# Kernel tuning notes

Hardware: AMD Instinct MI355X
Metric: run time of the kernel (lower is better)

The kernel has to match this reference:

```python
import jax, jax.numpy as jnp
import numpy as np

NUM_HEADS = 12
HEAD_DIM = 64  # dim=768 // 12
SCALE = HEAD_DIM ** (-0.5)  # NOTE: original divides q by this -> multiplies by sqrt(head_dim)


def setup_inputs() -> dict:
    key = jax.random.key(0)
    k1, k2, k3 = jax.random.split(key, 3)
    B, N, C = 1, 4096, 768
    x = jax.random.normal(k1, (B, N, C), dtype=jnp.float32)
    qkv_w = jax.random.normal(k2, (3 * C, C), dtype=jnp.float32) * 0.01
    qkv_b = jnp.zeros((3 * C,), dtype=jnp.float32)
    proj_w = jax.random.normal(k3, (C, C), dtype=jnp.float32) * 0.01
    proj_b = jnp.zeros((C,), dtype=jnp.float32)
    return {"x": x, "qkv_w": qkv_w, "qkv_b": qkv_b, "proj_w": proj_w, "proj_b": proj_b}


def reference(x, qkv_w, qkv_b, proj_w, proj_b):
    B, N, C = x.shape
    H, D = NUM_HEADS, HEAD_DIM
    # qkv projection: [B,N,3C]
    qkv = x @ qkv_w.T + qkv_b
    qkv = qkv.reshape(B, N, 3, H, D).transpose(2, 0, 3, 1, 4)  # [3,B,H,N,D]
    q, k, v = qkv[0], qkv[1], qkv[2]
    # Faithful quirk: q / scale with scale = D**-0.5 => logits scaled by sqrt(D)
    attn = jnp.einsum('bhnd,bhmd->bhnm', q / SCALE, k)  # [B,H,N,N]
    attn = jax.nn.softmax(attn, axis=-1)
    # dropout omitted (eval mode / deterministic reference)
    out = jnp.einsum('bhnm,bhmd->bhnd', attn, v)  # [B,H,N,D]
    out = out.transpose(0, 2, 1, 3).reshape(B, N, C)
    out = out @ proj_w.T + proj_b
    return out
```

## Files before the change

### kernel.cpp

```cpp
#include <hip/hip_runtime.h>


typedef short bf16x8 __attribute__((ext_vector_type(8)));
typedef float f32x4 __attribute__((ext_vector_type(4)));
typedef unsigned short u16;
typedef unsigned int u32;

__device__ __forceinline__ u16 f2bf(float f) {
  u32 u = __float_as_uint(f);
  u = (u + 0x7fffu + ((u >> 16) & 1u)) >> 16;
  return (u16)u;
}

__device__ __forceinline__ u32 cvtpk(float a, float b) {
  u32 r;
  asm("v_cvt_pk_bf16_f32 %0, %1, %2" : "=v"(r) : "v"(a), "v"(b));
  return r;
}

__device__ __forceinline__ void gload16(const void* g, void* l) {
  __builtin_amdgcn_global_load_lds(
      (const __attribute__((address_space(1))) unsigned int*)g,
      (__attribute__((address_space(3))) unsigned int*)l, 16, 0, 0);
}

__device__ __forceinline__ void pl32swap(u32& x, u32& y) {
  asm("v_permlane32_swap_b32 %0, %1" : "+v"(x), "+v"(y));
}
__device__ __forceinline__ void pl16swap(u32& x, u32& y) {
  asm("v_permlane16_swap_b32 %0, %1" : "+v"(x), "+v"(y));
}

__global__ void cast3(const float* __restrict__ a, int na4,
                      const float* __restrict__ b, int nb4,
                      const float* __restrict__ c, int nc4,
                      u16* __restrict__ oa, u16* __restrict__ obp, u16* __restrict__ oc) {
  int i = blockIdx.x * blockDim.x + threadIdx.x;
  const float* src;
  u16* dst;
  int j = i;
  if (i < na4) { src = a; dst = oa; }
  else if (i < na4 + nb4) { src = b; dst = obp; j = i - na4; }
  else if (i < na4 + nb4 + nc4) { src = c; dst = oc; j = i - na4 - nb4; }
  else return;
  float4 v = ((const float4*)src)[j];
  ushort4 o;
  o.x = f2bf(v.x); o.y = f2bf(v.y); o.z = f2bf(v.z); o.w = f2bf(v.w);
  ((ushort4*)dst)[j] = o;
}

template <int MODE>
__global__ __launch_bounds__(256, 2) void gemm_bt(
    const u16* __restrict__ A, const u16* __restrict__ B,
    const float* __restrict__ bias,
    u16* __restrict__ qb, u16* __restrict__ kbuf, u16* __restrict__ vb,
    float* __restrict__ outp, int K, int N) {
  constexpr int TM = (MODE == 1) ? 64 : 128;
  constexpr int MI = TM / 32;
  __shared__ __align__(16) u16 As[TM * 32];
  __shared__ __align__(16) u16 Bs[128 * 32];
  const int tid = threadIdx.x, lane = tid & 63, w = tid >> 6;
  const int wr = w >> 1, wc = w & 1, quad = lane >> 4, l15 = lane & 15;
  const int m0 = blockIdx.y * TM, n0 = blockIdx.x * 128;

  f32x4 acc[MI][4];
#pragma unroll
  for (int i = 0; i < MI; ++i)
#pragma unroll
    for (int j = 0; j < 4; ++j) acc[i][j] = (f32x4){0.f, 0.f, 0.f, 0.f};

  for (int k0 = 0; k0 < K; k0 += 32) {
    __syncthreads();
#pragma unroll
    for (int i = 0; i < TM / 64; ++i) {
      int chunk = i * 256 + tid;
      int row = chunk >> 2, kc = chunk & 3;
      gload16(A + (size_t)(m0 + row) * K + k0 + kc * 8, (char*)As + chunk * 16);
    }
#pragma unroll
    for (int i = 0; i < 2; ++i) {
      int chunk = i * 256 + tid;
      int row = chunk >> 2, kc = chunk & 3;
      gload16(B + (size_t)(n0 + row) * K + k0 + kc * 8, (char*)Bs + chunk * 16);
    }
    __syncthreads();
    bf16x8 af[MI], bfr[4];
#pragma unroll
    for (int mi = 0; mi < MI; ++mi)
      af[mi] = *(const bf16x8*)&As[(wr * (TM / 2) + mi * 16 + l15) * 32 + quad * 8];
#pragma unroll
    for (int ni = 0; ni < 4; ++ni)
      bfr[ni] = *(const bf16x8*)&Bs[(wc * 64 + ni * 16 + l15) * 32 + quad * 8];
#pragma unroll
    for (int mi = 0; mi < MI; ++mi)
#pragma unroll
      for (int ni = 0; ni < 4; ++ni)
        acc[mi][ni] = __builtin_amdgcn_mfma_f32_16x16x32_bf16(af[mi], bfr[ni], acc[mi][ni], 0, 0, 0);
  }

#pragma unroll
  for (int mi = 0; mi < MI; ++mi) {
    int row = m0 + wr * (TM / 2) + mi * 16 + quad * 4;
#pragma unroll
    for (int ni = 0; ni < 4; ++ni) {
      int col = n0 + wc * 64 + ni * 16 + l15;
      float bv = bias[col];
      if (MODE == 0) {
        int t = col / 768;
        int rem = col - t * 768;
        int hh = rem >> 6, d = rem & 63;
        if (t == 2) {
          u16* dst = vb + (size_t)hh * 64 * 4096 + (size_t)d * 4096 + row;
          ushort4 pk;
          pk.x = f2bf(acc[mi][ni][0] + bv);
          pk.y = f2bf(acc[mi][ni][1] + bv);
          pk.z = f2bf(acc[mi][ni][2] + bv);
          pk.w = f2bf(acc[mi][ni][3] + bv);
          *(ushort4*)dst = pk;
        } else {
          u16* dst = (t == 0 ? qb : kbuf) + (size_t)hh * 4096 * 64 + d;
          float sc = (t == 0) ? 11.541560327111707f : 1.f;
#pragma unroll
          for (int r = 0; r < 4; ++r)
            dst[(size_t)(row + r) * 64] = f2bf((acc[mi][ni][r] + bv) * sc);
        }
      } else {
#pragma unroll
        for (int r = 0; r < 4; ++r)
          outp[(size_t)(row + r) * N + col] = acc[mi][ni][r] + bv;
      }
    }
  }
}

__global__ __launch_bounds__(256, 3) void flash_attn(
    const u16* __restrict__ qb, const u16* __restrict__ kb,
    const u16* __restrict__ vtg, u16* __restrict__ ob) {
  __shared__ __align__(16) u16 Ks[2][64 * 64];
  __shared__ __align__(16) u16 Vs[2][64 * 64];

  const int b = blockIdx.x;
  const int g = (b & 7) * 96 + (b >> 3);
  const int h = g >> 6;
  const int q0 = (g & 63) * 64;

  const int tid = threadIdx.x, lane = tid & 63, w = tid >> 6;
  const int quad = lane >> 4, l15 = lane & 15;
  const int qh2 = w >> 1, kh = w & 1;
  const u16* qptr = qb + (size_t)h * 4096 * 64;
  const u16* kptr = kb + (size_t)h * 4096 * 64;
  const u16* vptr = vtg + (size_t)h * 64 * 4096;
  const int sw = l15 & 7;
  const int u0 = (quad ^ sw) * 8;
  const int u1 = ((quad + 4) ^ sw) * 8;
  const int uv = (((kh << 2) + quad) ^ sw) * 8;

  int c0 = w * 64 + lane, c1 = 256 + w * 64 + lane;
  int r0s = c0 >> 3, j0s = ((c0 & 7) ^ (r0s & 7)) * 8;
  int r1s = c1 >> 3, j1s = ((c1 & 7) ^ (r1s & 7)) * 8;

  bf16x8 qf[2][2];
#pragma unroll
  for (int qt = 0; qt < 2; ++qt)
#pragma unroll
    for (int c = 0; c < 2; ++c)
      qf[qt][c] = *(const bf16x8*)&qptr[(size_t)(q0 + qh2 * 32 + qt * 16 + l15) * 64 + c * 32 + quad * 8];

  f32x4 oacc[2][4];
  f32x4 lacc[2];
#pragma unroll
  for (int qt = 0; qt < 2; ++qt) {
    lacc[qt] = (f32x4){0.f, 0.f, 0.f, 0.f};
#pragma unroll
    for (int dt = 0; dt < 4; ++dt) oacc[qt][dt] = (f32x4){0.f, 0.f, 0.f, 0.f};
  }
  const f32x4 zero4 = (f32x4){0.f, 0.f, 0.f, 0.f};
  bf16x8 onesf;
#pragma unroll
  for (int i = 0; i < 8; ++i) onesf[i] = (short)0x3F80;

  bf16x8 pfprev[2], vprev[4];

  gload16(kptr + (size_t)r0s * 64 + j0s, (char*)&Ks[0][0] + c0 * 16);
  gload16(kptr + (size_t)r1s * 64 + j1s, (char*)&Ks[0][0] + c1 * 16);
  gload16(vptr + (size_t)r0s * 4096 + j0s, (char*)&Vs[0][0] + c0 * 16);
  gload16(vptr + (size_t)r1s * 4096 + j1s, (char*)&Vs[0][0] + c1 * 16);

  const u16* ks0 = kptr + (size_t)(64 + r0s) * 64 + j0s;
  const u16* ks1 = kptr + (size_t)(64 + r1s) * 64 + j1s;
  const u16* vs0 = vptr + (size_t)r0s * 4096 + 64 + j0s;
  const u16* vs1 = vptr + (size_t)r1s * 4096 + 64 + j1s;

  auto body = [&](int t, int buf) {
    __syncthreads();
    if (t < 63) {
      gload16(ks0, (char*)&Ks[buf ^ 1][0] + c0 * 16);
      gload16(ks1, (char*)&Ks[buf ^ 1][0] + c1 * 16);
      gload16(vs0, (char*)&Vs[buf ^ 1][0] + c0 * 16);
      gload16(vs1, (char*)&Vs[buf ^ 1][0] + c1 * 16);
      ks0 += 64 * 64; ks1 += 64 * 64; vs0 += 64; vs1 += 64;
    }

    bf16x8 kf[2][2];
#pragma unroll
    for (int mt = 0; mt < 2; ++mt) {
      const u16* kr = &Ks[buf][((kh << 5) + mt * 16 + l15) * 64];
      kf[mt][0] = *(const bf16x8*)(kr + u0);
      kf[mt][1] = *(const bf16x8*)(kr + u1);
    }

    __builtin_amdgcn_s_setprio(1);
    if (t > 0) {
#pragma unroll
      for (int qt = 0; qt < 2; ++qt) {
#pragma unroll
        for (int dt = 0; dt < 4; ++dt)
          oacc[qt][dt] = __builtin_amdgcn_mfma_f32_16x16x32_bf16(pfprev[qt], vprev[dt], oacc[qt][dt], 0, 0, 0);
        lacc[qt] = __builtin_amdgcn_mfma_f32_16x16x32_bf16(pfprev[qt], onesf, lacc[qt], 0, 0, 0);
      }
    }

    f32x4 st[2][2];
#pragma unroll
    for (int mt = 0; mt < 2; ++mt)
#pragma unroll
      for (int qt = 0; qt < 2; ++qt) {
        f32x4 z = __builtin_amdgcn_mfma_f32_16x16x32_bf16(kf[mt][0], qf[qt][0], zero4, 0, 0, 0);
        st[mt][qt] = __builtin_amdgcn_mfma_f32_16x16x32_bf16(kf[mt][1], qf[qt][1], z, 0, 0, 0);
      }
    __builtin_amdgcn_s_setprio(0);

#pragma unroll
    for (int dt = 0; dt < 4; ++dt)
      vprev[dt] = *(const bf16x8*)(&Vs[buf][(dt * 16 + l15) * 64] + uv);

#pragma unroll
    for (int qt = 0; qt < 2; ++qt) {
      float p00 = __builtin_amdgcn_exp2f(st[0][qt][0]);
      float p01 = __builtin_amdgcn_exp2f(st[0][qt][1]);
      float p02 = __builtin_amdgcn_exp2f(st[0][qt][2]);
      float p03 = __builtin_amdgcn_exp2f(st[0][qt][3]);
      float p10 = __builtin_amdgcn_exp2f(st[1][qt][0]);
      float p11 = __builtin_amdgcn_exp2f(st[1][qt][1]);
      float p12 = __builtin_amdgcn_exp2f(st[1][qt][2]);
      float p13 = __builtin_amdgcn_exp2f(st[1][qt][3]);
      u32 x0 = cvtpk(p00, p01), x1 = cvtpk(p02, p03);
      u32 y0 = cvtpk(p10, p11), y1 = cvtpk(p12, p13);
      pl32swap(x0, y0); pl16swap(x0, y0);
      pl32swap(x1, y1); pl16swap(x1, y1);
      union { u32 u[4]; bf16x8 v; } pu;
      pu.u[0] = x0; pu.u[1] = x1; pu.u[2] = y0; pu.u[3] = y1;
      pfprev[qt] = pu.v;
    }
  };

  for (int tt = 0; tt < 32; ++tt) {
    body(2 * tt, 0);
    body(2 * tt + 1, 1);
  }

#pragma unroll
  for (int qt = 0; qt < 2; ++qt) {
#pragma unroll
    for (int dt = 0; dt < 4; ++dt)
      oacc[qt][dt] = __builtin_amdgcn_mfma_f32_16x16x32_bf16(pfprev[qt], vprev[dt], oacc[qt][dt], 0, 0, 0);
    lacc[qt] = __builtin_amdgcn_mfma_f32_16x16x32_bf16(pfprev[qt], onesf, lacc[qt], 0, 0, 0);
  }

  __syncthreads();
  float* ored = (float*)&Ks[0][0];
  float* lred = (float*)&Vs[0][0];
  if (kh == 1) {
#pragma unroll
    for (int qt = 0; qt < 2; ++qt) {
#pragma unroll
      for (int dt = 0; dt < 4; ++dt)
        *(f32x4*)&ored[((((qh2 * 2 + qt) * 4 + dt) * 64) + lane) * 4] = oacc[qt][dt];
      if (l15 == 0) {
#pragma unroll
        for (int r = 0; r < 4; ++r)
          lred[(qh2 * 2 + qt) * 16 + quad * 4 + r] = lacc[qt][r];
      }
    }
  }
  __syncthreads();
  if (kh == 0) {
#pragma unroll
    for (int qt = 0; qt < 2; ++qt) {
      f32x4 linv;
#pragma unroll
      for (int r = 0; r < 4; ++r)
        linv[r] = 1.f / (lacc[qt][r] + lred[(qh2 * 2 + qt) * 16 + quad * 4 + r]);
#pragma unroll
      for (int dt = 0; dt < 4; ++dt) {
        f32x4 oo = *(const f32x4*)&ored[((((qh2 * 2 + qt) * 4 + dt) * 64) + lane) * 4];
        int row = q0 + qh2 * 32 + qt * 16 + quad * 4;
        u16* op = ob + (size_t)row * 768 + h * 64 + dt * 16 + l15;
        op[0]       = f2bf((oacc[qt][dt][0] + oo[0]) * linv[0]);
        op[768]     = f2bf((oacc[qt][dt][1] + oo[1]) * linv[1]);
        op[2 * 768] = f2bf((oacc[qt][dt][2] + oo[2]) * linv[2]);
        op[3 * 768] = f2bf((oacc[qt][dt][3] + oo[3]) * linv[3]);
      }
    }
  }
}

extern "C" void kernel_launch(void* const* d_in, const int* in_sizes, int n_in,
                              void* d_out, int out_size, void* d_ws, size_t ws_size,
                              hipStream_t stream) {
  const float* x      = (const float*)d_in[0];
  const float* qkv_w  = (const float*)d_in[1];
  const float* qkv_b  = (const float*)d_in[2];
  const float* proj_w = (const float*)d_in[3];
  const float* proj_b = (const float*)d_in[4];
  float* out = (float*)d_out;

  const int N = 4096, C = 768, H = 12, D = 64, C3 = 2304;
  char* ws = (char*)d_ws;
  size_t off = 0;
  u16* xb    = (u16*)(ws + off); off += (size_t)N * C * 2;
  u16* wqkv  = (u16*)(ws + off); off += (size_t)C3 * C * 2;
  u16* wproj = (u16*)(ws + off); off += (size_t)C * C * 2;
  u16* qbuf  = (u16*)(ws + off); off += (size_t)H * N * D * 2;
  u16* kbuf  = (u16*)(ws + off); off += (size_t)H * N * D * 2;
  u16* vbuf  = (u16*)(ws + off); off += (size_t)H * N * D * 2;
  u16* aob = xb;

  const int na4 = N * C / 4, nb4 = C3 * C / 4, nc4 = C * C / 4;
  int ntot = na4 + nb4 + nc4;
  cast3<<<(ntot + 255) / 256, 256, 0, stream>>>(x, na4, qkv_w, nb4, proj_w, nc4, xb, wqkv, wproj);

  dim3 g1(C3 / 128, N / 128);
  gemm_bt<0><<<g1, 256, 0, stream>>>(xb, wqkv, qkv_b, qbuf, kbuf, vbuf, nullptr, C, C3);

  flash_attn<<<768, 256, 0, stream>>>(qbuf, kbuf, vbuf, aob);

  dim3 g3(C / 128, N / 64);
  gemm_bt<1><<<g3, 256, 0, stream>>>(aob, wproj, proj_b, nullptr, nullptr, nullptr, out, C, C);
}
```

Measured before the change: 117.4 us.

## Load K tiles directly into registers, double-buffered, bypassing LDS

Removes the shared-memory K staging buffer. Each wave now fetches its own K MFMA fragments straight from global memory into two alternating register sets, one tile ahead of use. Only V still goes through LDS, and the final reduction scratch moves into the V buffer plus a small separate array. This is meant to cut LDS traffic and footprint and to drop the K ds_reads from the inner loop. In exchange it adds register pressure, duplicate global K loads across waves, and relies on the barrier's implicit vmcnt wait because the inline-asm loads are not tracked by the compiler.

New measurement: 156.1 us. 33.0% more time.

```diff
diff --git a/kernel.cpp b/kernel.cpp
--- a/kernel.cpp
+++ b/kernel.cpp
@@ -22,6 +22,10 @@
   __builtin_amdgcn_global_load_lds(
       (const __attribute__((address_space(1))) unsigned int*)g,
       (__attribute__((address_space(3))) unsigned int*)l, 16, 0, 0);
+}
+
+__device__ __forceinline__ void gld128(bf16x8& d, const u16* p) {
+  asm volatile("global_load_dwordx4 %0, %1, off" : "=v"(d) : "v"(p));
 }
 
 __device__ __forceinline__ void pl32swap(u32& x, u32& y) {
@@ -133,11 +137,61 @@
   }
 }
 
+#define FA_BODY(T, BUF, KU, KL)                                                              \
+  do {                                                                                       \
+    __syncthreads();                                                                         \
+    if ((T) < 63) {                                                                          \
+      gload16(vs0, (char*)&Vs[(BUF) ^ 1][0] + c0 * 16);                                      \
+      gload16(vs1, (char*)&Vs[(BUF) ^ 1][0] + c1 * 16);                                      \
+      vs0 += 64; vs1 += 64;                                                                  \
+      gld128(KL[0], kgn);                                                                    \
+      gld128(KL[1], kgn + 32);                                                               \
+      gld128(KL[2], kgn + 1024);                                                             \
+      gld128(KL[3], kgn + 1024 + 32);                                                        \
+      kgn += 4096;                                                                           \
+    }                                                                                        \
+    __builtin_amdgcn_s_setprio(1);                                                           \
+    if ((T) > 0) {                                                                           \
+      _Pragma("unroll") for (int qt = 0; qt < 2; ++qt) {                                     \
+        _Pragma("unroll") for (int dt = 0; dt < 4; ++dt)                                     \
+            oacc[qt][dt] = __builtin_amdgcn_mfma_f32_16x16x32_bf16(pfprev[qt], vprev[dt],    \
+                                                                   oacc[qt][dt], 0, 0, 0);  \
+        lacc[qt] = __builtin_amdgcn_mfma_f32_16x16x32_bf16(pfprev[qt], onesf, lacc[qt], 0, 0, 0); \
+      }                                                                                      \
+    }                                                                                        \
+    f32x4 st[2][2];                                                                          \
+    _Pragma("unroll") for (int mt = 0; mt < 2; ++mt)                                         \
+        _Pragma("unroll") for (int qt = 0; qt < 2; ++qt) {                                   \
+      f32x4 z = __builtin_amdgcn_mfma_f32_16x16x32_bf16(KU[mt * 2 + 0], qf[qt][0], zero4, 0, 0, 0); \
+      st[mt][qt] = __builtin_amdgcn_mfma_f32_16x16x32_bf16(KU[mt * 2 + 1], qf[qt][1], z, 0, 0, 0);  \
+    }                                                                                        \
+    __builtin_amdgcn_s_setprio(0);                                                           \
+    _Pragma("unroll") for (int dt = 0; dt < 4; ++dt)                                         \
+        vprev[dt] = *(const bf16x8*)(&Vs[BUF][(dt * 16 + l15) * 64] + uv);                   \
+    _Pragma("unroll") for (int qt = 0; qt < 2; ++qt) {                                       \
+      float p00 = __builtin_amdgcn_exp2f(st[0][qt][0]);                                      \
+      float p01 = __builtin_amdgcn_exp2f(st[0][qt][1]);                                      \
+      float p02 = __builtin_amdgcn_exp2f(st[0][qt][2]);                                      \
+      float p03 = __builtin_amdgcn_exp2f(st[0][qt][3]);                                      \
+      float p10 = __builtin_amdgcn_exp2f(st[1][qt][0]);                                      \
+      float p11 = __builtin_amdgcn_exp2f(st[1][qt][1]);                                      \
+      float p12 = __builtin_amdgcn_exp2f(st[1][qt][2]);                                      \
+      float p13 = __builtin_amdgcn_exp2f(st[1][qt][3]);                                      \
+      u32 x0 = cvtpk(p00, p01), x1 = cvtpk(p02, p03);                                        \
+      u32 y0 = cvtpk(p10, p11), y1 = cvtpk(p12, p13);                                        \
+      pl32swap(x0, y0); pl16swap(x0, y0);                                                    \
+      pl32swap(x1, y1); pl16swap(x1, y1);                                                    \
+      union { u32 u[4]; bf16x8 v; } pu;                                                      \
+      pu.u[0] = x0; pu.u[1] = x1; pu.u[2] = y0; pu.u[3] = y1;                                \
+      pfprev[qt] = pu.v;                                                                     \
+    }                                                                                        \
+  } while (0)
+
 __global__ __launch_bounds__(256, 3) void flash_attn(
     const u16* __restrict__ qb, const u16* __restrict__ kb,
     const u16* __restrict__ vtg, u16* __restrict__ ob) {
-  __shared__ __align__(16) u16 Ks[2][64 * 64];
   __shared__ __align__(16) u16 Vs[2][64 * 64];
+  __shared__ __align__(16) float lred[64];
 
   const int b = blockIdx.x;
   const int g = (b & 7) * 96 + (b >> 3);
@@ -151,14 +205,14 @@
   const u16* kptr = kb + (size_t)h * 4096 * 64;
   const u16* vptr = vtg + (size_t)h * 64 * 4096;
   const int sw = l15 & 7;
-  const int u0 = (quad ^ sw) * 8;
-  const int u1 = ((quad + 4) ^ sw) * 8;
   const int uv = (((kh << 2) + quad) ^ sw) * 8;
 
   int c0 = w * 64 + lane, c1 = 256 + w * 64 + lane;
   int r0s = c0 >> 3, j0s = ((c0 & 7) ^ (r0s & 7)) * 8;
   int r1s = c1 >> 3, j1s = ((c1 & 7) ^ (r1s & 7)) * 8;
 
+  const u16* kgn = kptr + (size_t)((kh << 5) + l15) * 64 + quad * 8;
+
   bf16x8 qf[2][2];
 #pragma unroll
   for (int qt = 0; qt < 2; ++qt)
@@ -180,83 +234,22 @@
   for (int i = 0; i < 8; ++i) onesf[i] = (short)0x3F80;
 
   bf16x8 pfprev[2], vprev[4];
-
-  gload16(kptr + (size_t)r0s * 64 + j0s, (char*)&Ks[0][0] + c0 * 16);
-  gload16(kptr + (size_t)r1s * 64 + j1s, (char*)&Ks[0][0] + c1 * 16);
+  bf16x8 knA[4], knB[4];
+
   gload16(vptr + (size_t)r0s * 4096 + j0s, (char*)&Vs[0][0] + c0 * 16);
   gload16(vptr + (size_t)r1s * 4096 + j1s, (char*)&Vs[0][0] + c1 * 16);
-
-  const u16* ks0 = kptr + (size_t)(64 + r0s) * 64 + j0s;
-  const u16* ks1 = kptr + (size_t)(64 + r1s) * 64 + j1s;
+  gld128(knA[0], kgn);
+  gld128(knA[1], kgn + 32);
+  gld128(knA[2], kgn + 1024);
+  gld128(knA[3], kgn + 1024 + 32);
+  kgn += 4096;
+
   const u16* vs0 = vptr + (size_t)r0s * 4096 + 64 + j0s;
   const u16* vs1 = vptr + (size_t)r1s * 4096 + 64 + j1s;
 
-  auto body = [&](int t, int buf) {
-    __syncthreads();
-    if (t < 63) {
-      gload16(ks0, (char*)&Ks[buf ^ 1][0] + c0 * 16);
-      gload16(ks1, (char*)&Ks[buf ^ 1][0] + c1 * 16);
-      gload16(vs0, (char*)&Vs[buf ^ 1][0] + c0 * 16);
-      gload16(vs1, (char*)&Vs[buf ^ 1][0] + c1 * 16);
-      ks0 += 64 * 64; ks1 += 64 * 64; vs0 += 64; vs1 += 64;
-    }
-
-    bf16x8 kf[2][2];
-#pragma unroll
-    for (int mt = 0; mt < 2; ++mt) {
-      const u16* kr = &Ks[buf][((kh << 5) + mt * 16 + l15) * 64];
-      kf[mt][0] = *(const bf16x8*)(kr + u0);
-      kf[mt][1] = *(const bf16x8*)(kr + u1);
-    }
-
-    __builtin_amdgcn_s_setprio(1);
-    if (t > 0) {
-#pragma unroll
-      for (int qt = 0; qt < 2; ++qt) {
-#pragma unroll
-        for (int dt = 0; dt < 4; ++dt)
-          oacc[qt][dt] = __builtin_amdgcn_mfma_f32_16x16x32_bf16(pfprev[qt], vprev[dt], oacc[qt][dt], 0, 0, 0);
-        lacc[qt] = __builtin_amdgcn_mfma_f32_16x16x32_bf16(pfprev[qt], onesf, lacc[qt], 0, 0, 0);
-      }
-    }
-
-    f32x4 st[2][2];
-#pragma unroll
-    for (int mt = 0; mt < 2; ++mt)
-#pragma unroll
-      for (int qt = 0; qt < 2; ++qt) {
-        f32x4 z = __builtin_amdgcn_mfma_f32_16x16x32_bf16(kf[mt][0], qf[qt][0], zero4, 0, 0, 0);
-        st[mt][qt] = __builtin_amdgcn_mfma_f32_16x16x32_bf16(kf[mt][1], qf[qt][1], z, 0, 0, 0);
-      }
-    __builtin_amdgcn_s_setprio(0);
-
-#pragma unroll
-    for (int dt = 0; dt < 4; ++dt)
-      vprev[dt] = *(const bf16x8*)(&Vs[buf][(dt * 16 + l15) * 64] + uv);
-
-#pragma unroll
-    for (int qt = 0; qt < 2; ++qt) {
-      float p00 = __builtin_amdgcn_exp2f(st[0][qt][0]);
-      float p01 = __builtin_amdgcn_exp2f(st[0][qt][1]);
-      float p02 = __builtin_amdgcn_exp2f(st[0][qt][2]);
-      float p03 = __builtin_amdgcn_exp2f(st[0][qt][3]);
-      float p10 = __builtin_amdgcn_exp2f(st[1][qt][0]);
-      float p11 = __builtin_amdgcn_exp2f(st[1][qt][1]);
-      float p12 = __builtin_amdgcn_exp2f(st[1][qt][2]);
-      float p13 = __builtin_amdgcn_exp2f(st[1][qt][3]);
-      u32 x0 = cvtpk(p00, p01), x1 = cvtpk(p02, p03);
-      u32 y0 = cvtpk(p10, p11), y1 = cvtpk(p12, p13);
-      pl32swap(x0, y0); pl16swap(x0, y0);
-      pl32swap(x1, y1); pl16swap(x1, y1);
-      union { u32 u[4]; bf16x8 v; } pu;
-      pu.u[0] = x0; pu.u[1] = x1; pu.u[2] = y0; pu.u[3] = y1;
-      pfprev[qt] = pu.v;
-    }
-  };
-
   for (int tt = 0; tt < 32; ++tt) {
-    body(2 * tt, 0);
-    body(2 * tt + 1, 1);
+    FA_BODY(2 * tt, 0, knA, knB);
+    FA_BODY(2 * tt + 1, 1, knB, knA);
   }
 
 #pragma unroll
@@ -268,8 +261,7 @@
   }
 
   __syncthreads();
-  float* ored = (float*)&Ks[0][0];
-  float* lred = (float*)&Vs[0][0];
+  float* ored = (float*)&Vs[0][0];
   if (kh == 1) {
 #pragma unroll
     for (int qt = 0; qt < 2; ++qt) {
```
